# Performance work log

Measured on AMD Instinct MI355X. Metric: run time of the kernel, lower is better.

Reference implementation:

```python
import jax, jax.numpy as jnp
import numpy as np

NUM_NODES = 100000
N = 65536          # subgraph nodes returned by LastNeighborLoader
E = 655360         # N * size(=10) last-neighbor edges
B = 4096           # temporal event batch
MEM = 128          # memory_dim (== pos_embedding_dim)
TIME = 64          # time_dim
MSG = 64           # raw_msg_dim
EMB = 128          # embedding_dim (gnn out_channels)
HEADS = 2
HD = EMB // HEADS  # 64, TransformerConv out_channels//2 per head
HID = 64           # mlp_hidden_dim[-1]
IN = 2 * MEM       # gnn in_channels (memory || pos memory)
EDGE_D = MSG + TIME


def setup_inputs() -> dict:
    key = jax.random.key(0)
    ks = jax.random.split(key, 32)
    nrm = lambda i, shp, s=1.0: jax.random.normal(ks[i], shp, jnp.float32) * s
    inp = {}
    # data / state tensors
    inp["memory"] = nrm(0, (NUM_NODES, MEM))
    inp["pos_memory"] = nrm(1, (NUM_NODES, MEM))
    inp["last_update"] = jax.random.uniform(ks[2], (NUM_NODES,), jnp.float32) * 1000.0
    inp["n_id"] = jnp.arange(N, dtype=jnp.int32)
    inp["edge_index"] = jax.random.randint(ks[3], (2, E), 0, N, dtype=jnp.int32)
    inp["edge_t"] = jax.random.uniform(ks[4], (E,), jnp.float32) * 1000.0
    inp["edge_msg"] = nrm(5, (E, MSG))
    inp["src"] = jax.random.randint(ks[6], (B,), 0, N, dtype=jnp.int32)
    inp["dst"] = jax.random.randint(ks[7], (B,), 0, N, dtype=jnp.int32)
    inp["neg_dst"] = jax.random.randint(ks[8], (B,), 0, N, dtype=jnp.int32)
    # learned parameters
    inp["time_w"] = nrm(9, (1, TIME))                      # TimeEncoder Linear(1, time_dim)
    inp["time_b"] = nrm(10, (TIME,), 0.1)
    sI = 1.0 / np.sqrt(IN); sE = 1.0 / np.sqrt(EDGE_D)
    inp["Wq"] = nrm(11, (IN, HEADS * HD), sI); inp["bq"] = jnp.zeros((HEADS * HD,), jnp.float32)
    inp["Wk"] = nrm(12, (IN, HEADS * HD), sI); inp["bk"] = jnp.zeros((HEADS * HD,), jnp.float32)
    inp["Wv"] = nrm(13, (IN, HEADS * HD), sI); inp["bv"] = jnp.zeros((HEADS * HD,), jnp.float32)
    inp["We"] = nrm(14, (EDGE_D, HEADS * HD), sE); inp["be"] = jnp.zeros((HEADS * HD,), jnp.float32)
    inp["Wskip"] = nrm(15, (IN, EMB), sI); inp["bskip"] = jnp.zeros((EMB,), jnp.float32)
    inp["mlp_w"] = nrm(16, (EMB, HID), 1.0 / np.sqrt(EMB)); inp["mlp_b"] = jnp.zeros((HID,), jnp.float32)
    sH = 1.0 / np.sqrt(HID)
    inp["lps_w"] = nrm(17, (HID, HID), sH); inp["lps_b"] = jnp.zeros((HID,), jnp.float32)
    inp["lpd_w"] = nrm(18, (HID, HID), sH); inp["lpd_b"] = jnp.zeros((HID,), jnp.float32)
    inp["lpf_w"] = nrm(19, (HID, 1), sH); inp["lpf_b"] = jnp.zeros((1,), jnp.float32)
    return inp


def reference(memory, pos_memory, last_update, n_id, edge_index, edge_t, edge_msg,
              src, dst, neg_dst, time_w, time_b, Wq, bq, Wk, bk, Wv, bv, We, be,
              Wskip, bskip, mlp_w, mlp_b, lps_w, lps_b, lpd_w, lpd_b, lpf_w, lpf_b):
    Nn = n_id.shape[0]
    # assoc remap: global node id -> local row in subgraph
    assoc = jnp.zeros((NUM_NODES,), jnp.int32).at[n_id].set(jnp.arange(Nn, dtype=jnp.int32))
    # memory read + positional memory concat  -> [N, 2*MEM]
    z = jnp.concatenate([memory[n_id], pos_memory[n_id]], axis=-1)
    lu = last_update[n_id]                                # [N]
    se, de = edge_index[0], edge_index[1]                 # source (j), target (i)
    # time encoding of relative time: cos(Linear(1->TIME))
    rel_t = lu[se] - edge_t                               # [E]
    t_enc = jnp.cos(rel_t[:, None] * time_w[0][None, :] + time_b)  # [E, TIME]
    edge_attr = jnp.concatenate([t_enc, edge_msg], axis=-1)        # [E, TIME+MSG]
    # TransformerConv (heads=2, concat): q from target, k/v from source (+edge)
    q = (z @ Wq + bq).reshape(Nn, HEADS, HD)
    k = (z @ Wk + bk).reshape(Nn, HEADS, HD)
    v = (z @ Wv + bv).reshape(Nn, HEADS, HD)
    e = (edge_attr @ We + be).reshape(-1, HEADS, HD)
    ke = k[se] + e                                        # [E, H, HD]
    ve = v[se] + e
    score = jnp.sum(q[de] * ke, axis=-1) / jnp.sqrt(jnp.float32(HD))  # [E, H]
    # segment softmax over incoming edges of each target node
    smax = jax.ops.segment_max(score, de, num_segments=Nn)
    ex = jnp.exp(score - smax[de])
    denom = jax.ops.segment_sum(ex, de, num_segments=Nn)
    alpha = ex / (denom[de] + 1e-16)                      # [E, H]
    agg = jax.ops.segment_sum(alpha[..., None] * ve, de, num_segments=Nn)  # [N, H, HD]
    out = agg.reshape(Nn, HEADS * HD) + (z @ Wskip + bskip)  # root/skip connection
    # MLP([embedding_dim, hidden]) -> single Linear (last layer: no act/norm)
    h = out @ mlp_w + mlp_b                               # [N, HID]
    z_src = h[assoc[src]]; z_dst = h[assoc[dst]]; z_neg = h[assoc[neg_dst]]
    def link_pred(a, b):
        hh = jax.nn.relu(a @ lps_w + lps_b + b @ lpd_w + lpd_b)
        return hh @ lpf_w + lpf_b
    pos_out = link_pred(z_src, z_dst)                     # [B, 1]
    neg_out = link_pred(z_src, z_neg)                     # [B, 1]
    return pos_out, neg_out
```

## Files before the change

kernel.cpp:

```cpp
#include <hip/hip_runtime.h>
#include <math.h>

#define NNODES 100000
#define NSUB   65536
#define NEDGE  655360
#define NBATCH 4096
#define LDK 72

typedef __attribute__((ext_vector_type(8))) short short8;
typedef __attribute__((ext_vector_type(4))) float f32x4;

__device__ __forceinline__ unsigned short f2bf(float x) {
  unsigned int b = __float_as_uint(x);
  b += 0x7fffu + ((b >> 16) & 1u);
  return (unsigned short)(b >> 16);
}
__device__ __forceinline__ float bf2f(unsigned short u) {
  return __uint_as_float(((unsigned int)u) << 16);
}
__device__ __forceinline__ float bflo(unsigned int u) { return __uint_as_float(u << 16); }
__device__ __forceinline__ float bfhi(unsigned int u) { return __uint_as_float(u & 0xffff0000u); }
__device__ __forceinline__ unsigned int pk2(float a, float b) {
  return (unsigned int)f2bf(a) | ((unsigned int)f2bf(b) << 16);
}
__device__ __forceinline__ void unpack8(uint4 u, float* a, float* b) {
  a[0] = bflo(u.x); b[0] = bfhi(u.x);
  a[1] = bflo(u.y); b[1] = bfhi(u.y);
  a[2] = bflo(u.z); b[2] = bfhi(u.z);
  a[3] = bflo(u.w); b[3] = bfhi(u.w);
}
__device__ __forceinline__ ushort4 pkv4(float a, float b, float c, float d) {
  return make_ushort4(f2bf(a), f2bf(b), f2bf(c), f2bf(d));
}

__global__ void k_sentinel(float* out) { out[0] = -12345.0f; }

__global__ void k_packW(const float* __restrict__ Wq, const float* __restrict__ bq,
                        const float* __restrict__ Wk, const float* __restrict__ bk,
                        const float* __restrict__ Wv, const float* __restrict__ bv,
                        const float* __restrict__ Ws, const float* __restrict__ bs,
                        const float* __restrict__ We,
                        unsigned short* __restrict__ Wt, float* __restrict__ bias) {
  int n = blockIdx.x, r = threadIdx.x;
  float v = 0.f, bn = 0.f;
  if (n < 128) {
    int l = n >> 1, h = n & 1;
    v = Wq[r * 128 + h * 64 + l] * 0.125f; bn = bq[h * 64 + l] * 0.125f;
  } else if (n < 256) {
    int i = n - 128, l = i >> 1, h = i & 1;
    v = Wk[r * 128 + h * 64 + l]; bn = bk[h * 64 + l];
  } else if (n < 384) {
    int i = n - 256, l = i >> 1, h = i & 1;
    v = Wv[r * 128 + h * 64 + l]; bn = bv[h * 64 + l];
  } else if (n < 512) {
    int c = n - 384; v = Ws[r * 128 + c]; bn = bs[c];
  } else {
    int i = (n < 640) ? (n - 512) : (n - 640);
    int c = i >> 1, h = i & 1;
    int kk = (n < 640) ? c : (64 + c);
    float s = 0.f;
    for (int d = 0; d < 64; d++) s += Wq[r * 128 + h * 64 + d] * We[kk * 128 + h * 64 + d];
    v = s * 0.125f;
    if (r == 0) {
      float sb = 0.f;
      for (int d = 0; d < 64; d++) sb += bq[h * 64 + d] * We[kk * 128 + h * 64 + d];
      bn = sb * 0.125f;
    }
  }
  Wt[(size_t)n * 256 + r] = f2bf(v);
  if (r == 0) bias[n] = bn;
}

__global__ void k_packW2(const float* __restrict__ We, const float* __restrict__ mlp_w,
                         unsigned short* __restrict__ W2t) {
  int r = blockIdx.x, j = threadIdx.x;
  float v;
  if (r < 128) v = mlp_w[r * 64 + j];
  else if (r < 192) { int k = r - 128; float s = 0; for (int c = 0; c < 64; c++) s += We[k * 128 + c] * mlp_w[c * 64 + j]; v = s; }
  else if (r < 256) { int k = r - 192; float s = 0; for (int c = 0; c < 64; c++) s += We[(64 + k) * 128 + c] * mlp_w[c * 64 + j]; v = s; }
  else if (r < 320) { int k = r - 256; float s = 0; for (int c = 0; c < 64; c++) s += We[k * 128 + 64 + c] * mlp_w[(64 + c) * 64 + j]; v = s; }
  else if (r < 384) { int k = r - 320; float s = 0; for (int c = 0; c < 64; c++) s += We[(64 + k) * 128 + 64 + c] * mlp_w[(64 + c) * 64 + j]; v = s; }
  else v = mlp_w[(r - 384) * 64 + j];
  W2t[(size_t)j * 512 + r] = f2bf(v);
}

__global__ void k_bem(const float* __restrict__ be, const float* __restrict__ mlp_w,
                      float* __restrict__ bem) {
  int h = blockIdx.x, j = threadIdx.x;
  float s = 0.f;
  for (int c = 0; c < 64; c++) s += be[h * 64 + c] * mlp_w[(h * 64 + c) * 64 + j];
  bem[h * 64 + j] = s;
}

__global__ void k_assoc(const int* __restrict__ n_id, int* __restrict__ assoc) {
  int i = blockIdx.x * 256 + threadIdx.x;
  if (i < NSUB) assoc[n_id[i]] = i;
}

__global__ void k_packA(const float* __restrict__ mem, const float* __restrict__ pmem,
                        const int* __restrict__ n_id, unsigned short* __restrict__ anodes) {
  int i = blockIdx.x * 256 + threadIdx.x;
  int node = i >> 5, ch = i & 31;
  int nid = n_id[node];
  const float* src = (ch < 16) ? (mem + (size_t)nid * 128 + ch * 8)
                               : (pmem + (size_t)nid * 128 + (ch - 16) * 8);
  float4 f0 = *(const float4*)src, f1 = *(const float4*)(src + 4);
  uint4 o;
  o.x = pk2(f0.x, f0.y); o.y = pk2(f0.z, f0.w);
  o.z = pk2(f1.x, f1.y); o.w = pk2(f1.z, f1.w);
  *(uint4*)(anodes + (size_t)node * 256 + ch * 8) = o;
}

__global__ void k_prep_edge(const int* __restrict__ edge_index, const int* __restrict__ n_id,
                            const float* __restrict__ last_update, const float* __restrict__ edge_t,
                            float* __restrict__ rel_t, int* __restrict__ deg) {
  int e = blockIdx.x * 256 + threadIdx.x;
  if (e < NEDGE) {
    rel_t[e] = last_update[n_id[edge_index[e]]] - edge_t[e];
    atomicAdd(&deg[edge_index[NEDGE + e]], 1);
  }
}

__global__ void k_msgb(const float* __restrict__ edge_msg, unsigned int* __restrict__ msgb) {
  int i = blockIdx.x * 256 + threadIdx.x;
  float2 f = *(const float2*)(edge_msg + (size_t)i * 2);
  msgb[i] = pk2(f.x, f.y);
}

__global__ __launch_bounds__(1024)
void k_scan1(const int* __restrict__ deg, int* __restrict__ excl, int* __restrict__ btot) {
  __shared__ int wsum[16];
  int t = threadIdx.x, w = t >> 6, l = t & 63;
  int i = blockIdx.x * 1024 + t;
  int v = deg[i], s = v;
  #pragma unroll
  for (int d = 1; d < 64; d <<= 1) { int u = __shfl_up(s, d, 64); if (l >= d) s += u; }
  if (l == 63) wsum[w] = s;
  __syncthreads();
  int woff = 0;
  #pragma unroll
  for (int k = 0; k < 16; k++) woff += (k < w) ? wsum[k] : 0;
  excl[i] = woff + s - v;
  if (t == 1023) btot[blockIdx.x] = woff + s;
}

__global__ void k_scan2(const int* __restrict__ btot, int* __restrict__ boff,
                        int* __restrict__ offs, int* __restrict__ cursor) {
  int l = threadIdx.x;
  int v = btot[l], s = v;
  #pragma unroll
  for (int d = 1; d < 64; d <<= 1) { int u = __shfl_up(s, d, 64); if (l >= d) s += u; }
  boff[l] = s - v;
  if (l == 63) { offs[NSUB] = s; cursor[NSUB] = s; }
}

__global__ __launch_bounds__(1024)
void k_scan3(const int* __restrict__ excl, const int* __restrict__ boff,
             int* __restrict__ offs, int* __restrict__ cursor) {
  int i = blockIdx.x * 1024 + threadIdx.x;
  int o = excl[i] + boff[blockIdx.x];
  offs[i] = o; cursor[i] = o;
}

__global__ void k_scatter(const int* __restrict__ edge_index, const float* __restrict__ rel_t,
                          int* __restrict__ cursor, uint4* __restrict__ csrmeta) {
  int e = blockIdx.x * 256 + threadIdx.x;
  if (e < NEDGE) {
    int de = edge_index[NEDGE + e];
    int p = atomicAdd(&cursor[de], 1);
    csrmeta[p] = make_uint4((unsigned)edge_index[e], __float_as_uint(rel_t[e]), (unsigned)e, 0u);
  }
}

__global__ __launch_bounds__(256)
void k_gemm_node(const unsigned short* __restrict__ anodes, const unsigned short* __restrict__ Wt,
                 const float* __restrict__ bias, unsigned short* __restrict__ nodeout) {
  __shared__ unsigned short sA[128][LDK];
  __shared__ unsigned short sB[128][LDK];
  int t = threadIdx.x;
  int row0 = blockIdx.x * 128, n0 = blockIdx.y * 128;
  int ar = t >> 1, ak = (t & 1) * 32;
  int w = t >> 6, lane = t & 63, quad = lane >> 4, r16 = lane & 15;
  int m_off = (w >> 1) * 64, n_off = (w & 1) * 64;
  f32x4 acc[4][4] = {};
  for (int st = 0; st < 4; st++) {
    int ks = st * 64;
    __syncthreads();
    #pragma unroll
    for (int i = 0; i < 4; i++)
      *(uint4*)&sA[ar][ak + i * 8] = *(const uint4*)(anodes + (size_t)(row0 + ar) * 256 + ks + ak + i * 8);
    #pragma unroll
    for (int i = 0; i < 4; i++)
      *(uint4*)&sB[ar][ak + i * 8] = *(const uint4*)(Wt + (size_t)(n0 + ar) * 256 + ks + ak + i * 8);
    __syncthreads();
    #pragma unroll
    for (int kk = 0; kk < 2; kk++) {
      short8 af[4], bf_[4];
      #pragma unroll
      for (int i = 0; i < 4; i++) af[i]  = *(const short8*)&sA[m_off + i * 16 + r16][kk * 32 + quad * 8];
      #pragma unroll
      for (int i = 0; i < 4; i++) bf_[i] = *(const short8*)&sB[n_off + i * 16 + r16][kk * 32 + quad * 8];
      #pragma unroll
      for (int i = 0; i < 4; i++)
        #pragma unroll
        for (int j = 0; j < 4; j++)
          acc[i][j] = __builtin_amdgcn_mfma_f32_16x16x32_bf16(af[i], bf_[j], acc[i][j], 0, 0, 0);
    }
  }
  #pragma unroll
  for (int j = 0; j < 4; j++) {
    int col = n0 + n_off + j * 16 + r16;
    float bv_ = bias[col];
    #pragma unroll
    for (int i = 0; i < 4; i++) {
      int rbase = row0 + m_off + i * 16 + quad * 4;
      #pragma unroll
      for (int rg = 0; rg < 4; rg++)
        nodeout[(size_t)(rbase + rg) * 768 + col] = f2bf(acc[i][j][rg] + bv_);
    }
  }
}

__global__ __launch_bounds__(256)
void k_edge(const unsigned short* __restrict__ nodeout, const unsigned short* __restrict__ msgb,
            const float* __restrict__ time_w, const float* __restrict__ time_b,
            const float* __restrict__ be, const int* __restrict__ offs,
            const uint4* __restrict__ csrmeta, unsigned short* __restrict__ aggbuf,
            float* __restrict__ salph) {
  int t = threadIdx.x, w = t >> 6, lane = t & 63;
  int j = lane & 15;
  int node = blockIdx.x * 16 + w * 4 + (lane >> 4);
  const unsigned short* nr = nodeout + (size_t)node * 768;
  uint4 q4  = *(const uint4*)(nr + 8 * j);
  uint4 qc4 = *(const uint4*)(nr + 512 + 8 * j);
  uint4 qm4 = *(const uint4*)(nr + 640 + 8 * j);
  float4 tw4 = *(const float4*)(time_w + 4 * j);
  float4 tb4 = *(const float4*)(time_b + 4 * j);
  float4 beA = *(const float4*)(be + 4 * j);
  float4 beB = *(const float4*)(be + 64 + 4 * j);
  float q0[4], q1[4], qc0[4], qc1[4], qm0[4], qm1[4];
  unpack8(q4, q0, q1); unpack8(qc4, qc0, qc1); unpack8(qm4, qm0, qm1);
  float qbe0 = q0[0] * beA.x + q0[1] * beA.y + q0[2] * beA.z + q0[3] * beA.w;
  float qbe1 = q1[0] * beB.x + q1[1] * beB.y + q1[2] * beB.z + q1[3] * beB.w;
  #pragma unroll
  for (int s = 1; s < 16; s <<= 1) { qbe0 += __shfl_xor(qbe0, s, 64); qbe1 += __shfl_xor(qbe1, s, 64); }
  float d0 = 0.f, d1 = 0.f;
  float aV0[4] = {}, aV1[4] = {}, aC0[4] = {}, aC1[4] = {}, aM0[4] = {}, aM1[4] = {};
  int e0 = offs[node], e1 = offs[node + 1];
  int deg = e1 - e0;
  int lb = lane & 48;
  for (int base = 0; base < deg; base += 16) {
    int cidx = e0 + base + j;
    int hi = e1 - 1;
    cidx = cidx > hi ? hi : cidx;
    uint4 mt = csrmeta[cidx];
    int rem = deg - base; rem = rem > 16 ? 16 : rem;
    for (int c = 0; c < rem; c += 4) {
      uint4 kvr[4], vvr[4];
      uint2 mgr[4];
      float rtv[4];
      #pragma unroll
      for (int ii = 0; ii < 4; ii++) {
        int sl = lb | (c + ii);
        int se_i = __shfl((int)mt.x, sl, 64);
        rtv[ii] = __uint_as_float((unsigned)__shfl((int)mt.y, sl, 64));
        int eid_i = __shfl((int)mt.z, sl, 64);
        const unsigned short* ns = nodeout + (size_t)se_i * 768;
        kvr[ii] = *(const uint4*)(ns + 128 + 8 * j);
        vvr[ii] = *(const uint4*)(ns + 256 + 8 * j);
        mgr[ii] = *(const uint2*)(msgb + (size_t)eid_i * 64 + 4 * j);
      }
      #pragma unroll
      for (int ii = 0; ii < 4; ii++) {
        float msk = (c + ii < rem) ? 1.f : 0.f;
        float k0[4], k1[4], v0[4], v1[4];
        unpack8(kvr[ii], k0, k1); unpack8(vvr[ii], v0, v1);
        float mgc[4] = {bflo(mgr[ii].x), bfhi(mgr[ii].x), bflo(mgr[ii].y), bfhi(mgr[ii].y)};
        float rt = rtv[ii];
        float cv[4];
        cv[0] = __cosf(rt * tw4.x + tb4.x);
        cv[1] = __cosf(rt * tw4.y + tb4.y);
        cv[2] = __cosf(rt * tw4.z + tb4.z);
        cv[3] = __cosf(rt * tw4.w + tb4.w);
        float p0 = q0[0] * k0[0] + q0[1] * k0[1] + q0[2] * k0[2] + q0[3] * k0[3]
                 + qc0[0] * cv[0] + qc0[1] * cv[1] + qc0[2] * cv[2] + qc0[3] * cv[3]
                 + qm0[0] * mgc[0] + qm0[1] * mgc[1] + qm0[2] * mgc[2] + qm0[3] * mgc[3];
        float p1 = q1[0] * k1[0] + q1[1] * k1[1] + q1[2] * k1[2] + q1[3] * k1[3]
                 + qc1[0] * cv[0] + qc1[1] * cv[1] + qc1[2] * cv[2] + qc1[3] * cv[3]
                 + qm1[0] * mgc[0] + qm1[1] * mgc[1] + qm1[2] * mgc[2] + qm1[3] * mgc[3];
        #pragma unroll
        for (int s = 1; s < 16; s <<= 1) { p0 += __shfl_xor(p0, s, 64); p1 += __shfl_xor(p1, s, 64); }
        float ex0 = __expf(p0 + qbe0) * msk, ex1 = __expf(p1 + qbe1) * msk;
        d0 += ex0; d1 += ex1;
        #pragma unroll
        for (int cc = 0; cc < 4; cc++) {
          aV0[cc] += ex0 * v0[cc]; aC0[cc] += ex0 * cv[cc]; aM0[cc] += ex0 * mgc[cc];
          aV1[cc] += ex1 * v1[cc]; aC1[cc] += ex1 * cv[cc]; aM1[cc] += ex1 * mgc[cc];
        }
      }
    }
  }
  float i0 = 1.f / (d0 + 1e-16f), i1 = 1.f / (d1 + 1e-16f);
  unsigned short* ag = aggbuf + (size_t)node * 512;
  *(ushort4*)(ag + 4 * j)       = pkv4(aV0[0] * i0, aV0[1] * i0, aV0[2] * i0, aV0[3] * i0);
  *(ushort4*)(ag + 64 + 4 * j)  = pkv4(aV1[0] * i1, aV1[1] * i1, aV1[2] * i1, aV1[3] * i1);
  *(ushort4*)(ag + 128 + 4 * j) = pkv4(aC0[0] * i0, aC0[1] * i0, aC0[2] * i0, aC0[3] * i0);
  *(ushort4*)(ag + 192 + 4 * j) = pkv4(aM0[0] * i0, aM0[1] * i0, aM0[2] * i0, aM0[3] * i0);
  *(ushort4*)(ag + 256 + 4 * j) = pkv4(aC1[0] * i1, aC1[1] * i1, aC1[2] * i1, aC1[3] * i1);
  *(ushort4*)(ag + 320 + 4 * j) = pkv4(aM1[0] * i1, aM1[1] * i1, aM1[2] * i1, aM1[3] * i1);
  *(uint4*)(ag + 384 + 8 * j)   = *(const uint4*)(nr + 384 + 8 * j);
  if (j == 0) { salph[node * 2] = d0 * i0; salph[node * 2 + 1] = d1 * i1; }
}

__global__ __launch_bounds__(128)
void k_gemm_final(const unsigned short* __restrict__ aggbuf, const unsigned short* __restrict__ W2t,
                  const float* __restrict__ salph, const float* __restrict__ bem,
                  const float* __restrict__ mlp_b, float* __restrict__ h) {
  __shared__ unsigned short sA[128][LDK];
  __shared__ unsigned short sB[64][LDK];
  int t = threadIdx.x;
  int row0 = blockIdx.x * 128;
  int w = t >> 6, lane = t & 63, quad = lane >> 4, r16 = lane & 15;
  int m_off = w * 64;
  f32x4 acc[4][4] = {};
  for (int st = 0; st < 8; st++) {
    int ks = st * 64;
    __syncthreads();
    #pragma unroll
    for (int c = 0; c < 8; c++)
      *(uint4*)&sA[t][c * 8] = *(const uint4*)(aggbuf + (size_t)(row0 + t) * 512 + ks + c * 8);
    int brr = t >> 1;
    #pragma unroll
    for (int jj = 0; jj < 4; jj++) {
      int c = (t & 1) * 4 + jj;
      *(uint4*)&sB[brr][c * 8] = *(const uint4*)(W2t + (size_t)brr * 512 + ks + c * 8);
    }
    __syncthreads();
    #pragma unroll
    for (int kk = 0; kk < 2; kk++) {
      short8 af[4], bf_[4];
      #pragma unroll
      for (int i = 0; i < 4; i++) af[i]  = *(const short8*)&sA[m_off + i * 16 + r16][kk * 32 + quad * 8];
      #pragma unroll
      for (int i = 0; i < 4; i++) bf_[i] = *(const short8*)&sB[i * 16 + r16][kk * 32 + quad * 8];
      #pragma unroll
      for (int i = 0; i < 4; i++)
        #pragma unroll
        for (int jj = 0; jj < 4; jj++)
          acc[i][jj] = __builtin_amdgcn_mfma_f32_16x16x32_bf16(af[i], bf_[jj], acc[i][jj], 0, 0, 0);
    }
  }
  #pragma unroll
  for (int jj = 0; jj < 4; jj++) {
    int col = jj * 16 + r16;
    float mb = mlp_b[col], b0 = bem[col], b1 = bem[64 + col];
    #pragma unroll
    for (int i = 0; i < 4; i++) {
      int rbase = row0 + m_off + i * 16 + quad * 4;
      #pragma unroll
      for (int rg = 0; rg < 4; rg++) {
        int rr = rbase + rg;
        h[(size_t)rr * 64 + col] = acc[i][jj][rg] + mb + salph[rr * 2] * b0 + salph[rr * 2 + 1] * b1;
      }
    }
  }
}

__global__ __launch_bounds__(256)
void k_linkpred(const float* __restrict__ h, const int* __restrict__ assoc,
                const int* __restrict__ src, const int* __restrict__ dst,
                const int* __restrict__ neg, const float* __restrict__ lps_w,
                const float* __restrict__ lps_b, const float* __restrict__ lpd_w,
                const float* __restrict__ lpd_b, const float* __restrict__ lpf_w,
                const float* __restrict__ lpf_b, float* __restrict__ out) {
  int t = threadIdx.x, w = t >> 6, j = t & 63;
  int b = blockIdx.x * 4 + w;
  const float* hs = h + (size_t)assoc[src[b]] * 64;
  const float* hd = h + (size_t)assoc[dst[b]] * 64;
  const float* hn = h + (size_t)assoc[neg[b]] * 64;
  float vs = lps_b[j], vd = lpd_b[j], vn = lpd_b[j];
  for (int k = 0; k < 64; k++) {
    float ws_ = lps_w[k * 64 + j];
    float wd_ = lpd_w[k * 64 + j];
    vs += hs[k] * ws_;
    vd += hd[k] * wd_;
    vn += hn[k] * wd_;
  }
  float fw = lpf_w[j];
  float hp = fmaxf(vs + vd, 0.f) * fw;
  float hq = fmaxf(vs + vn, 0.f) * fw;
  #pragma unroll
  for (int m = 1; m < 64; m <<= 1) {
    hp += __shfl_xor(hp, m, 64);
    hq += __shfl_xor(hq, m, 64);
  }
  if (j == 0) {
    out[b] = hp + lpf_b[0];
    out[NBATCH + b] = hq + lpf_b[0];
  }
}

extern "C" void kernel_launch(void* const* d_in, const int* in_sizes, int n_in,
                              void* d_out, int out_size, void* d_ws, size_t ws_size,
                              hipStream_t stream) {
  if (n_in < 30) return;
  const float* memory      = (const float*)d_in[0];
  const float* pos_memory  = (const float*)d_in[1];
  const float* last_update = (const float*)d_in[2];
  const int*   n_id        = (const int*)d_in[3];
  const int*   edge_index  = (const int*)d_in[4];
  const float* edge_t      = (const float*)d_in[5];
  const float* edge_msg    = (const float*)d_in[6];
  const int*   src         = (const int*)d_in[7];
  const int*   dst         = (const int*)d_in[8];
  const int*   neg_dst     = (const int*)d_in[9];
  const float* time_w      = (const float*)d_in[10];
  const float* time_b      = (const float*)d_in[11];
  const float* Wq = (const float*)d_in[12]; const float* bq = (const float*)d_in[13];
  const float* Wk = (const float*)d_in[14]; const float* bk = (const float*)d_in[15];
  const float* Wv = (const float*)d_in[16]; const float* bv = (const float*)d_in[17];
  const float* We = (const float*)d_in[18]; const float* be = (const float*)d_in[19];
  const float* Wskip = (const float*)d_in[20]; const float* bskip = (const float*)d_in[21];
  const float* mlp_w = (const float*)d_in[22]; const float* mlp_b = (const float*)d_in[23];
  const float* lps_w = (const float*)d_in[24]; const float* lps_b = (const float*)d_in[25];
  const float* lpd_w = (const float*)d_in[26]; const float* lpd_b = (const float*)d_in[27];
  const float* lpf_w = (const float*)d_in[28]; const float* lpf_b = (const float*)d_in[29];
  float* out = (float*)d_out;

  char* ws = (char*)d_ws;
  size_t off = 0;
  auto alloc = [&](size_t bytes) -> void* {
    void* p = ws + off;
    off += (bytes + 255) & ~(size_t)255;
    return p;
  };
  int*   assoc   = (int*)alloc((size_t)NNODES * 4);
  unsigned short* Wt  = (unsigned short*)alloc((size_t)768 * 256 * 2);
  float* bias    = (float*)alloc(768 * 4);
  unsigned short* W2t = (unsigned short*)alloc((size_t)64 * 512 * 2);
  float* bem     = (float*)alloc(128 * 4);
  float* rel_t   = (float*)alloc((size_t)NEDGE * 4);
  unsigned short* anodes  = (unsigned short*)alloc((size_t)NSUB * 256 * 2);
  unsigned short* nodeout = (unsigned short*)alloc((size_t)NSUB * 768 * 2);
  unsigned short* aggbuf  = (unsigned short*)alloc((size_t)NSUB * 512 * 2);
  float* salph   = (float*)alloc((size_t)NSUB * 2 * 4);
  int*   deg     = (int*)alloc((size_t)NSUB * 4);
  int*   offs    = (int*)alloc((size_t)(NSUB + 1) * 4);
  int*   cursor  = (int*)alloc((size_t)(NSUB + 1) * 4);
  int*   excl    = (int*)alloc((size_t)NSUB * 4);
  int*   btot    = (int*)alloc(64 * 4);
  int*   boff    = (int*)alloc(64 * 4);
  uint4* csrmeta = (uint4*)alloc((size_t)NEDGE * 16);
  unsigned int* msgb = (unsigned int*)alloc((size_t)NEDGE * 64 * 2);
  float* hbuf    = (float*)alloc((size_t)NSUB * 64 * 4);

  if (ws_size < off) {
    k_sentinel<<<1, 1, 0, stream>>>(out);
    return;
  }

  (void)hipMemsetAsync(deg, 0, (size_t)NSUB * 4, stream);
  k_packW<<<768, 256, 0, stream>>>(Wq, bq, Wk, bk, Wv, bv, Wskip, bskip, We, Wt, bias);
  k_packW2<<<512, 64, 0, stream>>>(We, mlp_w, W2t);
  k_bem<<<2, 64, 0, stream>>>(be, mlp_w, bem);
  k_assoc<<<NSUB / 256, 256, 0, stream>>>(n_id, assoc);
  k_packA<<<NSUB * 32 / 256, 256, 0, stream>>>(memory, pos_memory, n_id, anodes);
  k_prep_edge<<<NEDGE / 256, 256, 0, stream>>>(edge_index, n_id, last_update, edge_t, rel_t, deg);
  k_msgb<<<NEDGE * 32 / 256, 256, 0, stream>>>(edge_msg, msgb);
  k_scan1<<<NSUB / 1024, 1024, 0, stream>>>(deg, excl, btot);
  k_scan2<<<1, 64, 0, stream>>>(btot, boff, offs, cursor);
  k_scan3<<<NSUB / 1024, 1024, 0, stream>>>(excl, boff, offs, cursor);
  k_scatter<<<NEDGE / 256, 256, 0, stream>>>(edge_index, rel_t, cursor, csrmeta);
  k_gemm_node<<<dim3(NSUB / 128, 6), 256, 0, stream>>>(anodes, Wt, bias, nodeout);
  k_edge<<<NSUB / 16, 256, 0, stream>>>(nodeout, (const unsigned short*)msgb, time_w, time_b,
                                        be, offs, csrmeta, aggbuf, salph);
  k_gemm_final<<<NSUB / 128, 128, 0, stream>>>(aggbuf, W2t, salph, bem, mlp_b, hbuf);
  k_linkpred<<<NBATCH / 4, 256, 0, stream>>>(hbuf, assoc, src, dst, neg_dst,
                                             lps_w, lps_b, lpd_w, lpd_b, lpf_w, lpf_b, out);
}
```

Measured before the change: 698.7 us.

## Fuse prep kernels, merge scans, interleave K/V rows, enlarge node GEMM tile

Merges the three weight-packing kernels into one launch, folds the assoc build into the node-feature pack kernel, and folds edge prep into the message-conversion kernel. The block-offset scan is now recomputed inside the final scan pass, so that launch and its buffer go away. K and V weight rows are interleaved in groups of 8, so each edge gathers its key and value slices from one contiguous 32-byte span. The node GEMM tile doubles to 256 rows to reuse each B tile across more rows, at the cost of more registers and LDS per block.

```diff
diff --git a/kernel.cpp b/kernel.cpp
--- a/kernel.cpp
+++ b/kernel.cpp
@@ -15,9 +15,6 @@
   b += 0x7fffu + ((b >> 16) & 1u);
   return (unsigned short)(b >> 16);
 }
-__device__ __forceinline__ float bf2f(unsigned short u) {
-  return __uint_as_float(((unsigned int)u) << 16);
-}
 __device__ __forceinline__ float bflo(unsigned int u) { return __uint_as_float(u << 16); }
 __device__ __forceinline__ float bfhi(unsigned int u) { return __uint_as_float(u & 0xffff0000u); }
 __device__ __forceinline__ unsigned int pk2(float a, float b) {
@@ -35,71 +32,69 @@
 
 __global__ void k_sentinel(float* out) { out[0] = -12345.0f; }
 
-__global__ void k_packW(const float* __restrict__ Wq, const float* __restrict__ bq,
-                        const float* __restrict__ Wk, const float* __restrict__ bk,
-                        const float* __restrict__ Wv, const float* __restrict__ bv,
-                        const float* __restrict__ Ws, const float* __restrict__ bs,
-                        const float* __restrict__ We,
-                        unsigned short* __restrict__ Wt, float* __restrict__ bias) {
-  int n = blockIdx.x, r = threadIdx.x;
-  float v = 0.f, bn = 0.f;
-  if (n < 128) {
-    int l = n >> 1, h = n & 1;
-    v = Wq[r * 128 + h * 64 + l] * 0.125f; bn = bq[h * 64 + l] * 0.125f;
-  } else if (n < 256) {
-    int i = n - 128, l = i >> 1, h = i & 1;
-    v = Wk[r * 128 + h * 64 + l]; bn = bk[h * 64 + l];
-  } else if (n < 384) {
-    int i = n - 256, l = i >> 1, h = i & 1;
-    v = Wv[r * 128 + h * 64 + l]; bn = bv[h * 64 + l];
-  } else if (n < 512) {
-    int c = n - 384; v = Ws[r * 128 + c]; bn = bs[c];
+__global__ void k_packAll(const float* __restrict__ Wq, const float* __restrict__ bq,
+                          const float* __restrict__ Wk, const float* __restrict__ bk,
+                          const float* __restrict__ Wv, const float* __restrict__ bv,
+                          const float* __restrict__ Ws, const float* __restrict__ bs,
+                          const float* __restrict__ We, const float* __restrict__ mlp_w,
+                          const float* __restrict__ be,
+                          unsigned short* __restrict__ Wt, float* __restrict__ bias,
+                          unsigned short* __restrict__ W2t, float* __restrict__ bem) {
+  int b = blockIdx.x, t = threadIdx.x;
+  if (b < 768) {
+    int n = b, r = t;
+    float v = 0.f, bn = 0.f;
+    if (n < 128) {
+      int l = n >> 1, h = n & 1;
+      v = Wq[r * 128 + h * 64 + l] * 0.125f; bn = bq[h * 64 + l] * 0.125f;
+    } else if (n < 384) {
+      int p = n - 128, jj = p >> 4, r2 = p & 15;
+      if (r2 < 8) { int i = jj * 8 + r2; int l = i >> 1, h = i & 1;
+        v = Wk[r * 128 + h * 64 + l]; bn = bk[h * 64 + l]; }
+      else { int i = jj * 8 + (r2 - 8); int l = i >> 1, h = i & 1;
+        v = Wv[r * 128 + h * 64 + l]; bn = bv[h * 64 + l]; }
+    } else if (n < 512) {
+      int c = n - 384; v = Ws[r * 128 + c]; bn = bs[c];
+    } else {
+      int i = (n < 640) ? (n - 512) : (n - 640);
+      int c = i >> 1, h = i & 1;
+      int kk = (n < 640) ? c : (64 + c);
+      float s = 0.f;
+      for (int d = 0; d < 64; d++) s += Wq[r * 128 + h * 64 + d] * We[kk * 128 + h * 64 + d];
+      v = s * 0.125f;
+      if (r == 0) {
+        float sb = 0.f;
+        for (int d = 0; d < 64; d++) sb += bq[h * 64 + d] * We[kk * 128 + h * 64 + d];
+        bn = sb * 0.125f;
+      }
+    }
+    Wt[(size_t)n * 256 + r] = f2bf(v);
+    if (r == 0) bias[n] = bn;
+  } else if (b < 896) {
+    int r = (b - 768) * 4 + (t >> 6), j = t & 63;
+    float v;
+    if (r < 128) v = mlp_w[r * 64 + j];
+    else if (r < 192) { int k = r - 128; float s = 0; for (int c = 0; c < 64; c++) s += We[k * 128 + c] * mlp_w[c * 64 + j]; v = s; }
+    else if (r < 256) { int k = r - 192; float s = 0; for (int c = 0; c < 64; c++) s += We[(64 + k) * 128 + c] * mlp_w[c * 64 + j]; v = s; }
+    else if (r < 320) { int k = r - 256; float s = 0; for (int c = 0; c < 64; c++) s += We[k * 128 + 64 + c] * mlp_w[(64 + c) * 64 + j]; v = s; }
+    else if (r < 384) { int k = r - 320; float s = 0; for (int c = 0; c < 64; c++) s += We[(64 + k) * 128 + 64 + c] * mlp_w[(64 + c) * 64 + j]; v = s; }
+    else v = mlp_w[(r - 384) * 64 + j];
+    W2t[(size_t)j * 512 + r] = f2bf(v);
   } else {
-    int i = (n < 640) ? (n - 512) : (n - 640);
-    int c = i >> 1, h = i & 1;
-    int kk = (n < 640) ? c : (64 + c);
-    float s = 0.f;
-    for (int d = 0; d < 64; d++) s += Wq[r * 128 + h * 64 + d] * We[kk * 128 + h * 64 + d];
-    v = s * 0.125f;
-    if (r == 0) {
-      float sb = 0.f;
-      for (int d = 0; d < 64; d++) sb += bq[h * 64 + d] * We[kk * 128 + h * 64 + d];
-      bn = sb * 0.125f;
-    }
-  }
-  Wt[(size_t)n * 256 + r] = f2bf(v);
-  if (r == 0) bias[n] = bn;
-}
-
-__global__ void k_packW2(const float* __restrict__ We, const float* __restrict__ mlp_w,
-                         unsigned short* __restrict__ W2t) {
-  int r = blockIdx.x, j = threadIdx.x;
-  float v;
-  if (r < 128) v = mlp_w[r * 64 + j];
-  else if (r < 192) { int k = r - 128; float s = 0; for (int c = 0; c < 64; c++) s += We[k * 128 + c] * mlp_w[c * 64 + j]; v = s; }
-  else if (r < 256) { int k = r - 192; float s = 0; for (int c = 0; c < 64; c++) s += We[(64 + k) * 128 + c] * mlp_w[c * 64 + j]; v = s; }
-  else if (r < 320) { int k = r - 256; float s = 0; for (int c = 0; c < 64; c++) s += We[k * 128 + 64 + c] * mlp_w[(64 + c) * 64 + j]; v = s; }
-  else if (r < 384) { int k = r - 320; float s = 0; for (int c = 0; c < 64; c++) s += We[(64 + k) * 128 + 64 + c] * mlp_w[(64 + c) * 64 + j]; v = s; }
-  else v = mlp_w[(r - 384) * 64 + j];
-  W2t[(size_t)j * 512 + r] = f2bf(v);
-}
-
-__global__ void k_bem(const float* __restrict__ be, const float* __restrict__ mlp_w,
-                      float* __restrict__ bem) {
-  int h = blockIdx.x, j = threadIdx.x;
-  float s = 0.f;
-  for (int c = 0; c < 64; c++) s += be[h * 64 + c] * mlp_w[(h * 64 + c) * 64 + j];
-  bem[h * 64 + j] = s;
-}
-
-__global__ void k_assoc(const int* __restrict__ n_id, int* __restrict__ assoc) {
+    if (t < 64) {
+      int h = b - 896, j = t;
+      float s = 0.f;
+      for (int c = 0; c < 64; c++) s += be[h * 64 + c] * mlp_w[(h * 64 + c) * 64 + j];
+      bem[h * 64 + j] = s;
+    }
+  }
+}
+
+__global__ void k_packA(const float* __restrict__ mem, const float* __restrict__ pmem,
+                        const int* __restrict__ n_id, unsigned short* __restrict__ anodes,
+                        int* __restrict__ assoc) {
   int i = blockIdx.x * 256 + threadIdx.x;
   if (i < NSUB) assoc[n_id[i]] = i;
-}
-
-__global__ void k_packA(const float* __restrict__ mem, const float* __restrict__ pmem,
-                        const int* __restrict__ n_id, unsigned short* __restrict__ anodes) {
-  int i = blockIdx.x * 256 + threadIdx.x;
   int node = i >> 5, ch = i & 31;
   int nid = n_id[node];
   const float* src = (ch < 16) ? (mem + (size_t)nid * 128 + ch * 8)
@@ -111,20 +106,17 @@
   *(uint4*)(anodes + (size_t)node * 256 + ch * 8) = o;
 }
 
-__global__ void k_prep_edge(const int* __restrict__ edge_index, const int* __restrict__ n_id,
-                            const float* __restrict__ last_update, const float* __restrict__ edge_t,
-                            float* __restrict__ rel_t, int* __restrict__ deg) {
-  int e = blockIdx.x * 256 + threadIdx.x;
-  if (e < NEDGE) {
-    rel_t[e] = last_update[n_id[edge_index[e]]] - edge_t[e];
-    atomicAdd(&deg[edge_index[NEDGE + e]], 1);
-  }
-}
-
-__global__ void k_msgb(const float* __restrict__ edge_msg, unsigned int* __restrict__ msgb) {
+__global__ void k_msgb(const float* __restrict__ edge_msg, unsigned int* __restrict__ msgb,
+                       const int* __restrict__ edge_index, const int* __restrict__ n_id,
+                       const float* __restrict__ last_update, const float* __restrict__ edge_t,
+                       float* __restrict__ rel_t, int* __restrict__ deg) {
   int i = blockIdx.x * 256 + threadIdx.x;
   float2 f = *(const float2*)(edge_msg + (size_t)i * 2);
   msgb[i] = pk2(f.x, f.y);
+  if (i < NEDGE) {
+    rel_t[i] = last_update[n_id[edge_index[i]]] - edge_t[i];
+    atomicAdd(&deg[edge_index[NEDGE + i]], 1);
+  }
 }
 
 __global__ __launch_bounds__(1024)
@@ -144,22 +136,19 @@
   if (t == 1023) btot[blockIdx.x] = woff + s;
 }
 
-__global__ void k_scan2(const int* __restrict__ btot, int* __restrict__ boff,
-                        int* __restrict__ offs, int* __restrict__ cursor) {
-  int l = threadIdx.x;
+__global__ __launch_bounds__(1024)
+void k_scan3(const int* __restrict__ excl, const int* __restrict__ btot,
+             int* __restrict__ offs, int* __restrict__ cursor) {
+  int t = threadIdx.x, l = t & 63;
+  int bid = blockIdx.x;
   int v = btot[l], s = v;
   #pragma unroll
   for (int d = 1; d < 64; d <<= 1) { int u = __shfl_up(s, d, 64); if (l >= d) s += u; }
-  boff[l] = s - v;
-  if (l == 63) { offs[NSUB] = s; cursor[NSUB] = s; }
-}
-
-__global__ __launch_bounds__(1024)
-void k_scan3(const int* __restrict__ excl, const int* __restrict__ boff,
-             int* __restrict__ offs, int* __restrict__ cursor) {
-  int i = blockIdx.x * 1024 + threadIdx.x;
-  int o = excl[i] + boff[blockIdx.x];
+  int boff = __shfl(s, bid, 64) - __shfl(v, bid, 64);
+  int i = bid * 1024 + t;
+  int o = excl[i] + boff;
   offs[i] = o; cursor[i] = o;
+  if (bid == 63 && t == 1023) { offs[NSUB] = s; cursor[NSUB] = s; }
 }
 
 __global__ void k_scatter(const int* __restrict__ edge_index, const float* __restrict__ rel_t,
@@ -175,33 +164,33 @@
 __global__ __launch_bounds__(256)
 void k_gemm_node(const unsigned short* __restrict__ anodes, const unsigned short* __restrict__ Wt,
                  const float* __restrict__ bias, unsigned short* __restrict__ nodeout) {
-  __shared__ unsigned short sA[128][LDK];
+  __shared__ unsigned short sA[256][LDK];
   __shared__ unsigned short sB[128][LDK];
   int t = threadIdx.x;
-  int row0 = blockIdx.x * 128, n0 = blockIdx.y * 128;
+  int row0 = blockIdx.x * 256, n0 = blockIdx.y * 128;
   int ar = t >> 1, ak = (t & 1) * 32;
   int w = t >> 6, lane = t & 63, quad = lane >> 4, r16 = lane & 15;
-  int m_off = (w >> 1) * 64, n_off = (w & 1) * 64;
-  f32x4 acc[4][4] = {};
+  int m_off = (w >> 1) * 128, n_off = (w & 1) * 64;
+  f32x4 acc[8][4] = {};
   for (int st = 0; st < 4; st++) {
     int ks = st * 64;
     __syncthreads();
     #pragma unroll
-    for (int i = 0; i < 4; i++)
-      *(uint4*)&sA[ar][ak + i * 8] = *(const uint4*)(anodes + (size_t)(row0 + ar) * 256 + ks + ak + i * 8);
-    #pragma unroll
-    for (int i = 0; i < 4; i++)
-      *(uint4*)&sB[ar][ak + i * 8] = *(const uint4*)(Wt + (size_t)(n0 + ar) * 256 + ks + ak + i * 8);
+    for (int i = 0; i < 4; i++) {
+      *(uint4*)&sA[ar][ak + i * 8]       = *(const uint4*)(anodes + (size_t)(row0 + ar) * 256 + ks + ak + i * 8);
+      *(uint4*)&sA[ar + 128][ak + i * 8] = *(const uint4*)(anodes + (size_t)(row0 + ar + 128) * 256 + ks + ak + i * 8);
+      *(uint4*)&sB[ar][ak + i * 8]       = *(const uint4*)(Wt + (size_t)(n0 + ar) * 256 + ks + ak + i * 8);
+    }
     __syncthreads();
     #pragma unroll
     for (int kk = 0; kk < 2; kk++) {
-      short8 af[4], bf_[4];
-      #pragma unroll
-      for (int i = 0; i < 4; i++) af[i]  = *(const short8*)&sA[m_off + i * 16 + r16][kk * 32 + quad * 8];
+      short8 af[8], bf_[4];
+      #pragma unroll
+      for (int i = 0; i < 8; i++) af[i]  = *(const short8*)&sA[m_off + i * 16 + r16][kk * 32 + quad * 8];
       #pragma unroll
       for (int i = 0; i < 4; i++) bf_[i] = *(const short8*)&sB[n_off + i * 16 + r16][kk * 32 + quad * 8];
       #pragma unroll
-      for (int i = 0; i < 4; i++)
+      for (int i = 0; i < 8; i++)
         #pragma unroll
         for (int j = 0; j < 4; j++)
           acc[i][j] = __builtin_amdgcn_mfma_f32_16x16x32_bf16(af[i], bf_[j], acc[i][j], 0, 0, 0);
@@ -212,7 +201,7 @@
     int col = n0 + n_off + j * 16 + r16;
     float bv_ = bias[col];
     #pragma unroll
-    for (int i = 0; i < 4; i++) {
+    for (int i = 0; i < 8; i++) {
       int rbase = row0 + m_off + i * 16 + quad * 4;
       #pragma unroll
       for (int rg = 0; rg < 4; rg++)
@@ -266,8 +255,8 @@
         rtv[ii] = __uint_as_float((unsigned)__shfl((int)mt.y, sl, 64));
         int eid_i = __shfl((int)mt.z, sl, 64);
         const unsigned short* ns = nodeout + (size_t)se_i * 768;
-        kvr[ii] = *(const uint4*)(ns + 128 + 8 * j);
-        vvr[ii] = *(const uint4*)(ns + 256 + 8 * j);
+        kvr[ii] = *(const uint4*)(ns + 128 + 16 * j);
+        vvr[ii] = *(const uint4*)(ns + 128 + 16 * j + 8);
         mgr[ii] = *(const uint2*)(msgb + (size_t)eid_i * 64 + 4 * j);
       }
       #pragma unroll
@@ -449,7 +438,6 @@
   int*   cursor  = (int*)alloc((size_t)(NSUB + 1) * 4);
   int*   excl    = (int*)alloc((size_t)NSUB * 4);
   int*   btot    = (int*)alloc(64 * 4);
-  int*   boff    = (int*)alloc(64 * 4);
   uint4* csrmeta = (uint4*)alloc((size_t)NEDGE * 16);
   unsigned int* msgb = (unsigned int*)alloc((size_t)NEDGE * 64 * 2);
   float* hbuf    = (float*)alloc((size_t)NSUB * 64 * 4);
@@ -460,18 +448,15 @@
   }
 
   (void)hipMemsetAsync(deg, 0, (size_t)NSUB * 4, stream);
-  k_packW<<<768, 256, 0, stream>>>(Wq, bq, Wk, bk, Wv, bv, Wskip, bskip, We, Wt, bias);
-  k_packW2<<<512, 64, 0, stream>>>(We, mlp_w, W2t);
-  k_bem<<<2, 64, 0, stream>>>(be, mlp_w, bem);
-  k_assoc<<<NSUB / 256, 256, 0, stream>>>(n_id, assoc);
-  k_packA<<<NSUB * 32 / 256, 256, 0, stream>>>(memory, pos_memory, n_id, anodes);
-  k_prep_edge<<<NEDGE / 256, 256, 0, stream>>>(edge_index, n_id, last_update, edge_t, rel_t, deg);
-  k_msgb<<<NEDGE * 32 / 256, 256, 0, stream>>>(edge_msg, msgb);
+  k_packAll<<<898, 256, 0, stream>>>(Wq, bq, Wk, bk, Wv, bv, Wskip, bskip, We, mlp_w, be,
+                                     Wt, bias, W2t, bem);
+  k_packA<<<NSUB * 32 / 256, 256, 0, stream>>>(memory, pos_memory, n_id, anodes, assoc);
+  k_msgb<<<NEDGE * 32 / 256, 256, 0, stream>>>(edge_msg, msgb, edge_index, n_id,
+                                               last_update, edge_t, rel_t, deg);
   k_scan1<<<NSUB / 1024, 1024, 0, stream>>>(deg, excl, btot);
-  k_scan2<<<1, 64, 0, stream>>>(btot, boff, offs, cursor);
-  k_scan3<<<NSUB / 1024, 1024, 0, stream>>>(excl, boff, offs, cursor);
+  k_scan3<<<NSUB / 1024, 1024, 0, stream>>>(excl, btot, offs, cursor);
   k_scatter<<<NEDGE / 256, 256, 0, stream>>>(edge_index, rel_t, cursor, csrmeta);
-  k_gemm_node<<<dim3(NSUB / 128, 6), 256, 0, stream>>>(anodes, Wt, bias, nodeout);
+  k_gemm_node<<<dim3(NSUB / 256, 6), 256, 0, stream>>>(anodes, Wt, bias, nodeout);
   k_edge<<<NSUB / 16, 256, 0, stream>>>(nodeout, (const unsigned short*)msgb, time_w, time_b,
                                         be, offs, csrmeta, aggbuf, salph);
   k_gemm_final<<<NSUB / 128, 128, 0, stream>>>(aggbuf, W2t, salph, bem, mlp_b, hbuf);
```

Result: no change. 708.0 us (+1.3%).
